# Kernel tuning notes

Hardware: AMD Instinct MI355X
Metric: run time of the kernel (lower is better)

## Reference

```python
import jax, jax.numpy as jnp
import numpy as np

EXPERT_NUM = 8
TOPK = 2
N_EMBD = 768
D_FF = 3072
B, S = 2, 1024
T = B * S


def setup_inputs() -> dict:
    key = jax.random.key(0)
    ks = jax.random.split(key, 6)
    x = jax.random.normal(ks[0], (B, S, N_EMBD), dtype=jnp.float32)
    # gumbel noise, matching gumbel_noise(n, k) in the torch module
    u = jax.random.uniform(ks[1], (T, EXPERT_NUM), dtype=jnp.float32,
                           minval=1e-6, maxval=1.0 - 1e-6)
    noise = -jnp.log(-jnp.log(u))
    router_w = jax.random.normal(ks[2], (EXPERT_NUM, N_EMBD), dtype=jnp.float32) * (N_EMBD ** -0.5)
    w1 = jax.random.normal(ks[3], (EXPERT_NUM, N_EMBD, D_FF), dtype=jnp.float32) * (N_EMBD ** -0.5)
    b1 = jnp.zeros((EXPERT_NUM, D_FF), dtype=jnp.float32)
    w2 = jax.random.normal(ks[4], (EXPERT_NUM, D_FF, N_EMBD), dtype=jnp.float32) * (D_FF ** -0.5)
    b2 = jnp.zeros((EXPERT_NUM, N_EMBD), dtype=jnp.float32)
    return {"x": x, "noise": noise, "router_w": router_w,
            "w1": w1, "b1": b1, "w2": w2, "b2": b2}


def reference(x, noise, router_w, w1, b1, w2, b2):
    d = x.shape[-1]
    xs = x.reshape(-1, d)                                   # [T, d]
    gate_logits = xs @ router_w.T + noise                   # [T, E]
    # topk_exp > 1 branch: topk first, then softmax over the k kept logits
    weights, selected = jax.lax.top_k(gate_logits, TOPK)    # [T, k]
    weights = jax.nn.softmax(weights.astype(jnp.float32), axis=1).astype(x.dtype)
    out = jnp.zeros_like(xs)
    for e in range(EXPERT_NUM):
        # combine weight of expert e per token (0 where not selected)
        w_e = jnp.sum(jnp.where(selected == e, weights, 0.0), axis=1)  # [T]
        h = jax.nn.gelu(xs @ w1[e] + b1[e])                 # [T, d_ff]
        y = h @ w2[e] + b2[e]                               # [T, d]
        out = out + w_e[:, None] * y
    return out.reshape(x.shape)
```

## Files before the change

kernel.cpp:

```cpp
#include <hip/hip_runtime.h>
#include <hip/hip_bf16.h>

#define T_TOK 2048
#define NE 768
#define DFF 3072
#define NEXP 8
#define ROWS_PAD 4480
#define MAX_TILES 40

typedef __attribute__((ext_vector_type(8))) __bf16 bf16x8;
typedef __attribute__((ext_vector_type(4))) __bf16 bf16x4;
typedef __attribute__((ext_vector_type(4))) float f32x4;

__device__ __forceinline__ float gelu_tanh(float v) {
  float u = 0.7978845608028654f * (v + 0.044715f * v * v * v);
  float e = __expf(-2.0f * fabsf(u));
  float t = (1.0f - e) / (1.0f + e);
  t = copysignf(t, u);
  return 0.5f * v * (1.0f + t);
}

__global__ void router_kernel(const float* __restrict__ x,
                              const float* __restrict__ noise,
                              const float* __restrict__ rw,
                              int* __restrict__ sel, float* __restrict__ wgt) {
  int tok  = (blockIdx.x * blockDim.x + threadIdx.x) >> 6;
  int lane = threadIdx.x & 63;
  const float* xr = x + (size_t)tok * NE;
  float acc[NEXP];
#pragma unroll
  for (int e = 0; e < NEXP; e++) acc[e] = 0.f;
  for (int d = lane; d < NE; d += 64) {
    float xv = xr[d];
#pragma unroll
    for (int e = 0; e < NEXP; e++) acc[e] += xv * rw[e * NE + d];
  }
#pragma unroll
  for (int e = 0; e < NEXP; e++) {
#pragma unroll
    for (int off = 32; off > 0; off >>= 1) acc[e] += __shfl_xor(acc[e], off);
  }
  if (lane == 0) {
    float lg[NEXP];
#pragma unroll
    for (int e = 0; e < NEXP; e++) lg[e] = acc[e] + noise[tok * NEXP + e];
    int i0 = 0;
#pragma unroll
    for (int e = 1; e < NEXP; e++) if (lg[e] > lg[i0]) i0 = e;
    int i1 = (i0 == 0) ? 1 : 0;
#pragma unroll
    for (int e = 0; e < NEXP; e++) if (e != i0 && lg[e] > lg[i1]) i1 = e;
    float ex = __expf(lg[i1] - lg[i0]);
    float w0 = 1.f / (1.f + ex);
    sel[tok * 2]     = i0; sel[tok * 2 + 1] = i1;
    wgt[tok * 2]     = w0; wgt[tok * 2 + 1] = 1.f - w0;
  }
}

__global__ void assign_kernel(const int* __restrict__ sel,
                              int* __restrict__ offs, int* __restrict__ pair_tok,
                              int* __restrict__ slot_of, int* __restrict__ tiles,
                              int* __restrict__ ntl) {
  __shared__ int scnt[NEXP];
  __shared__ int soff[NEXP + 1];
  int e = threadIdx.x >> 6;
  int lane = threadIdx.x & 63;

  int count = 0;
  for (int t0 = 0; t0 < T_TOK; t0 += 64) {
    int t = t0 + lane;
    bool m = (sel[t * 2] == e) | (sel[t * 2 + 1] == e);
    count += __popcll(__ballot(m));
  }
  if (lane == 0) scnt[e] = count;
  __syncthreads();

  if (threadIdx.x == 0) {
    int s = 0;
    for (int k = 0; k < NEXP; k++) { soff[k] = s; s += scnt[k]; }
    soff[NEXP] = s;
    for (int i = 0; i <= NEXP; i++) offs[i] = soff[i];
    int k2 = 0;
    for (int k = 0; k < NEXP; k++)
      for (int r = soff[k]; r < soff[k + 1]; r += 128) {
        tiles[k2 * 2] = k; tiles[k2 * 2 + 1] = r; k2++;
      }
    *ntl = k2;
  }
  __syncthreads();

  int base = soff[e];
  for (int t0 = 0; t0 < T_TOK; t0 += 64) {
    int t = t0 + lane;
    int s0 = sel[t * 2], s1 = sel[t * 2 + 1];
    bool m0 = (s0 == e), m1 = (s1 == e);
    bool m = m0 | m1;
    unsigned long long mask = __ballot(m);
    int pos = __popcll(mask & ((1ull << lane) - 1ull));
    if (m) {
      int slot = base + pos;
      pair_tok[slot] = t;
      slot_of[t * 2 + (m0 ? 0 : 1)] = slot;
    }
    base += __popcll(mask);
  }
}

__global__ void gather_kernel(const float* __restrict__ x, const int* __restrict__ pair_tok,
                              __hip_bfloat16* __restrict__ xg) {
  int r = blockIdx.x;
  int tok = pair_tok[r];
  const float4* s = (const float4*)(x + (size_t)tok * NE);
  __hip_bfloat16* d = xg + (size_t)r * NE;
  int t = threadIdx.x;
  if (t < NE / 4) {
    float4 v = s[t];
    bf16x4 o;
    o[0] = (__bf16)__float2bfloat16(v.x); o[1] = (__bf16)__float2bfloat16(v.y);
    o[2] = (__bf16)__float2bfloat16(v.z); o[3] = (__bf16)__float2bfloat16(v.w);
    *reinterpret_cast<bf16x4*>(&d[t * 4]) = o;
  }
}

__global__ void transpose_cvt(const float* __restrict__ src, __hip_bfloat16* __restrict__ dst,
                              int K, int N) {
  __shared__ __hip_bfloat16 tile[64 * 72];
  int ntk = K >> 6, ntn = N >> 6;
  int bid = blockIdx.x;
  int e = bid / (ntk * ntn);
  int rem = bid % (ntk * ntn);
  int tk = rem / ntn, tn = rem % ntn;
  const float* s = src + (size_t)e * K * N + (size_t)(tk * 64) * N + tn * 64;
  int t = threadIdx.x;
  int a = t & 15;
  int kp = t >> 4;
#pragma unroll
  for (int i = 0; i < 2; i++) {
    int k = 2 * kp + 32 * i;
    float4 v0 = *reinterpret_cast<const float4*>(&s[(size_t)k * N + 4 * a]);
    float4 v1 = *reinterpret_cast<const float4*>(&s[(size_t)(k + 1) * N + 4 * a]);
    const float* p0 = &v0.x; const float* p1 = &v1.x;
#pragma unroll
    for (int j = 0; j < 4; j++) {
      __hip_bfloat162 p;
      p.x = __float2bfloat16(p0[j]); p.y = __float2bfloat16(p1[j]);
      *reinterpret_cast<__hip_bfloat162*>(&tile[(4 * a + j) * 72 + k]) = p;
    }
  }
  __syncthreads();
  int n = t >> 3, g = t & 7;
  __hip_bfloat16* d = dst + (size_t)e * N * K + (size_t)(tn * 64) * K + tk * 64;
#pragma unroll
  for (int i = 0; i < 2; i++) {
    int row = n + 32 * i;
    bf16x8 v = *reinterpret_cast<const bf16x8*>(&tile[row * 72 + g * 8]);
    *reinterpret_cast<bf16x8*>(&d[(size_t)row * K + g * 8]) = v;
  }
}

template <int K, int N, int MODE, int SPLITS>
__global__ __launch_bounds__(256) void ffn_gemm(
    const __hip_bfloat16* __restrict__ A, const __hip_bfloat16* __restrict__ Bt,
    const float* __restrict__ bias, __hip_bfloat16* __restrict__ DST,
    const int* __restrict__ offs, const int* __restrict__ tiles,
    const int* __restrict__ ntl) {
  constexpr int NT = N / 128;
  constexpr int KS = K / SPLITS;
  constexpr int NS = KS / 64;
  int bid = blockIdx.x;
  int nt = bid % NT;
  int r1 = bid / NT;
  int sp = r1 % SPLITS;
  int ti = r1 / SPLITS;
  if (ti >= *ntl) return;
  int e = tiles[ti * 2], row0 = tiles[ti * 2 + 1];
  int rend = offs[e + 1];
  int n0 = nt * 128;
  int kbeg = sp * KS;

  __shared__ __align__(16) __hip_bfloat16 lds[2][2][128 * 64];

  int tid = threadIdx.x;
  int w = tid >> 6, l = tid & 63;
  int wr = w >> 1, wc = w & 1;
  int r16 = l & 15, q = l >> 4;
  int swz = r16 & 7;

  f32x4 acc[4][4];
#pragma unroll
  for (int m = 0; m < 4; m++)
#pragma unroll
    for (int n = 0; n < 4; n++) acc[m][n] = (f32x4){0.f, 0.f, 0.f, 0.f};

  const __hip_bfloat16* Bte = Bt + (size_t)e * N * K;

  auto STAGE = [&](int b, int k0) {
    char* cA = (char*)lds[b][0];
    char* cB = (char*)lds[b][1];
#pragma unroll
    for (int i = 0; i < 4; i++) {
      int c = tid + 256 * i;
      int row = c >> 3, p = c & 7;
      const __hip_bfloat16* ga =
          A + (size_t)(row0 + row) * K + k0 + ((p ^ (row & 7)) << 3);
      __builtin_amdgcn_global_load_lds(
          (const __attribute__((address_space(1))) void*)ga,
          (__attribute__((address_space(3))) void*)(cA + c * 16), 16, 0, 0);
    }
#pragma unroll
    for (int i = 0; i < 4; i++) {
      int c = tid + 256 * i;
      int row = c >> 3, p = c & 7;
      const __hip_bfloat16* gb =
          Bte + (size_t)(n0 + row) * K + k0 + ((p ^ (row & 7)) << 3);
      __builtin_amdgcn_global_load_lds(
          (const __attribute__((address_space(1))) void*)gb,
          (__attribute__((address_space(3))) void*)(cB + c * 16), 16, 0, 0);
    }
  };

  STAGE(0, kbeg);
  for (int t = 0; t < NS; t++) {
    if (t + 1 < NS) {
      STAGE((t + 1) & 1, kbeg + (t + 1) * 64);
      asm volatile("s_waitcnt vmcnt(8)" ::: "memory");
    } else {
      asm volatile("s_waitcnt vmcnt(0)" ::: "memory");
    }
    __builtin_amdgcn_s_barrier();
    __builtin_amdgcn_sched_barrier(0);
    const char* cA = (const char*)lds[t & 1][0];
    const char* cB = (const char*)lds[t & 1][1];
#pragma unroll
    for (int kk = 0; kk < 2; kk++) {
      int inner = ((kk * 4 + q) ^ swz) << 4;
      bf16x8 aF[4], bF[4];
#pragma unroll
      for (int m = 0; m < 4; m++)
        aF[m] = *reinterpret_cast<const bf16x8*>(cA + (wr * 64 + m * 16 + r16) * 128 + inner);
#pragma unroll
      for (int n = 0; n < 4; n++)
        bF[n] = *reinterpret_cast<const bf16x8*>(cB + (wc * 64 + n * 16 + r16) * 128 + inner);
#pragma unroll
      for (int m = 0; m < 4; m++)
#pragma unroll
        for (int n = 0; n < 4; n++)
          acc[m][n] = __builtin_amdgcn_mfma_f32_16x16x32_bf16(aF[m], bF[n], acc[m][n], 0, 0, 0);
    }
    __builtin_amdgcn_s_barrier();
  }

  float* ldsF = (float*)&lds[0][0][0];
  __hip_bfloat16* dst = DST + (size_t)sp * ROWS_PAD * N;
#pragma unroll
  for (int hh = 0; hh < 2; hh++) {
    __syncthreads();
    if (wr == hh) {
#pragma unroll
      for (int m = 0; m < 4; m++)
#pragma unroll
        for (int n = 0; n < 4; n++)
#pragma unroll
          for (int rg = 0; rg < 4; rg++)
            ldsF[(m * 16 + q * 4 + rg) * 132 + wc * 64 + n * 16 + r16] = acc[m][n][rg];
    }
    __syncthreads();
#pragma unroll
    for (int i = 0; i < 4; i++) {
      int s = tid + 256 * i;
      int r = s >> 4, c8 = s & 15;
      int rr = row0 + hh * 64 + r;
      if (rr < rend) {
        const float* src = &ldsF[r * 132 + c8 * 8];
        float4 v0 = *reinterpret_cast<const float4*>(src);
        float4 v1 = *reinterpret_cast<const float4*>(src + 4);
        const float* bp = &bias[e * N + n0 + c8 * 8];
        float4 bb0 = *reinterpret_cast<const float4*>(bp);
        float4 bb1 = *reinterpret_cast<const float4*>(bp + 4);
        float vv[8]  = {v0.x, v0.y, v0.z, v0.w, v1.x, v1.y, v1.z, v1.w};
        float bbv[8] = {bb0.x, bb0.y, bb0.z, bb0.w, bb1.x, bb1.y, bb1.z, bb1.w};
        bf16x8 o;
#pragma unroll
        for (int j = 0; j < 8; j++) {
          float val;
          if (MODE == 0) val = gelu_tanh(vv[j] + bbv[j]);
          else           val = vv[j] + (sp == 0 ? bbv[j] : 0.f);
          o[j] = (__bf16)__float2bfloat16(val);
        }
        *reinterpret_cast<bf16x8*>(&dst[(size_t)rr * N + n0 + c8 * 8]) = o;
      }
    }
  }
}

template <int SPLITS>
__global__ void combine_kernel(const __hip_bfloat16* __restrict__ yb,
                               const int* __restrict__ slot_of,
                               const float* __restrict__ wgt,
                               float* __restrict__ out) {
  int t = blockIdx.x;
  int d = threadIdx.x;
  int s0 = slot_of[2 * t], s1 = slot_of[2 * t + 1];
  float w0 = wgt[2 * t], w1 = wgt[2 * t + 1];
  float a0 = 0.f, a1 = 0.f, a2 = 0.f, a3 = 0.f;
#pragma unroll
  for (int sp = 0; sp < SPLITS; sp++) {
    bf16x4 p = reinterpret_cast<const bf16x4*>(yb + (size_t)(sp * ROWS_PAD + s0) * NE)[d];
    bf16x4 r = reinterpret_cast<const bf16x4*>(yb + (size_t)(sp * ROWS_PAD + s1) * NE)[d];
    a0 += w0 * (float)p[0] + w1 * (float)r[0];
    a1 += w0 * (float)p[1] + w1 * (float)r[1];
    a2 += w0 * (float)p[2] + w1 * (float)r[2];
    a3 += w0 * (float)p[3] + w1 * (float)r[3];
  }
  float4 o = {a0, a1, a2, a3};
  reinterpret_cast<float4*>(out)[(size_t)t * (NE / 4) + d] = o;
}

extern "C" void kernel_launch(void* const* d_in, const int* in_sizes, int n_in,
                              void* d_out, int out_size, void* d_ws, size_t ws_size,
                              hipStream_t stream) {
  const float* x     = (const float*)d_in[0];
  const float* noise = (const float*)d_in[1];
  const float* rw    = (const float*)d_in[2];
  const float* w1    = (const float*)d_in[3];
  const float* b1    = (const float*)d_in[4];
  const float* w2    = (const float*)d_in[5];
  const float* b2    = (const float*)d_in[6];
  float* out = (float*)d_out;

  constexpr int SP2 = 4;

  char* ws = (char*)d_ws;
  size_t off = 0;
  auto carve = [&](size_t bytes) { void* p = ws + off; off = (off + bytes + 255) & ~255ull; return p; };
  int*   offs     = (int*)carve((NEXP + 1) * 4);
  int*   sel      = (int*)carve(T_TOK * 2 * 4);
  float* wgt      = (float*)carve(T_TOK * 2 * 4);
  int*   pair_tok = (int*)carve(ROWS_PAD * 4);
  int*   slot_of  = (int*)carve(T_TOK * 2 * 4);
  int*   tiles    = (int*)carve(MAX_TILES * 2 * 4);
  int*   ntl      = (int*)carve(4);
  __hip_bfloat16* xg  = (__hip_bfloat16*)carve((size_t)ROWS_PAD * NE * 2);
  __hip_bfloat16* h   = (__hip_bfloat16*)carve((size_t)ROWS_PAD * DFF * 2);
  __hip_bfloat16* yb  = (__hip_bfloat16*)carve((size_t)SP2 * ROWS_PAD * NE * 2);
  __hip_bfloat16* wt  = (__hip_bfloat16*)carve((size_t)NEXP * NE * DFF * 2);

  hipMemsetAsync(d_out, 0, (size_t)out_size * sizeof(float), stream);
  if (off > ws_size) return;

  router_kernel<<<(T_TOK * 64) / 256, 256, 0, stream>>>(x, noise, rw, sel, wgt);
  assign_kernel<<<1, 512, 0, stream>>>(sel, offs, pair_tok, slot_of, tiles, ntl);
  gather_kernel<<<T_TOK * 2, 256, 0, stream>>>(x, pair_tok, xg);

  transpose_cvt<<<NEXP * (NE / 64) * (DFF / 64), 256, 0, stream>>>(w1, wt, NE, DFF);
  ffn_gemm<NE, DFF, 0, 1><<<MAX_TILES * 1 * (DFF / 128), 256, 0, stream>>>(
      xg, wt, b1, h, offs, tiles, ntl);

  transpose_cvt<<<NEXP * (DFF / 64) * (NE / 64), 256, 0, stream>>>(w2, wt, DFF, NE);
  ffn_gemm<DFF, NE, 1, SP2><<<MAX_TILES * SP2 * (NE / 128), 256, 0, stream>>>(
      h, wt, b2, yb, offs, tiles, ntl);

  combine_kernel<SP2><<<T_TOK, 192, 0, stream>>>(yb, slot_of, wgt, out);
}
```

Before: 159.0 us.

## Switch FFN GEMM to triple-buffered 32-wide K stages, halve split-K

The grouped FFN GEMM now stages 32-wide K slices into a 3-deep LDS ring with an XOR chunk swizzle, where it used to stage 64-wide slices into a double buffer. This keeps two loads in flight per iteration to hide global latency while keeping LDS usage about the same. Split-K for the second GEMM drops from 4 to 2, which means less partial-sum traffic in combine but fewer blocks. The output memset now runs only on the early-exit path, because combine already writes every output element. Each iteration does half the MFMA work, so barrier overhead per FLOP doubles.

```diff
diff --git a/kernel.cpp b/kernel.cpp
--- a/kernel.cpp
+++ b/kernel.cpp
@@ -158,6 +158,10 @@
   }
 }
 
+__device__ __forceinline__ int swz_chunk(int c) {
+  return (c & ~7) | ((c & 7) ^ ((c >> 3) & 7));
+}
+
 template <int K, int N, int MODE, int SPLITS>
 __global__ __launch_bounds__(256) void ffn_gemm(
     const __hip_bfloat16* __restrict__ A, const __hip_bfloat16* __restrict__ Bt,
@@ -166,7 +170,7 @@
     const int* __restrict__ ntl) {
   constexpr int NT = N / 128;
   constexpr int KS = K / SPLITS;
-  constexpr int NS = KS / 64;
+  constexpr int NS = KS / 32;
   int bid = blockIdx.x;
   int nt = bid % NT;
   int r1 = bid / NT;
@@ -178,13 +182,12 @@
   int n0 = nt * 128;
   int kbeg = sp * KS;
 
-  __shared__ __align__(16) __hip_bfloat16 lds[2][2][128 * 64];
+  __shared__ __align__(16) __hip_bfloat16 lds[3][2][128 * 32];
 
   int tid = threadIdx.x;
   int w = tid >> 6, l = tid & 63;
   int wr = w >> 1, wc = w & 1;
   int r16 = l & 15, q = l >> 4;
-  int swz = r16 & 7;
 
   f32x4 acc[4][4];
 #pragma unroll
@@ -198,55 +201,58 @@
     char* cA = (char*)lds[b][0];
     char* cB = (char*)lds[b][1];
 #pragma unroll
-    for (int i = 0; i < 4; i++) {
-      int c = tid + 256 * i;
-      int row = c >> 3, p = c & 7;
-      const __hip_bfloat16* ga =
-          A + (size_t)(row0 + row) * K + k0 + ((p ^ (row & 7)) << 3);
+    for (int i = 0; i < 2; i++) {
+      int Lc = tid + 256 * i;
+      int fc = swz_chunk(Lc);
+      int row = fc >> 2, p = fc & 3;
+      const __hip_bfloat16* ga = A + (size_t)(row0 + row) * K + k0 + p * 8;
       __builtin_amdgcn_global_load_lds(
           (const __attribute__((address_space(1))) void*)ga,
-          (__attribute__((address_space(3))) void*)(cA + c * 16), 16, 0, 0);
-    }
-#pragma unroll
-    for (int i = 0; i < 4; i++) {
-      int c = tid + 256 * i;
-      int row = c >> 3, p = c & 7;
-      const __hip_bfloat16* gb =
-          Bte + (size_t)(n0 + row) * K + k0 + ((p ^ (row & 7)) << 3);
+          (__attribute__((address_space(3))) void*)(cA + Lc * 16), 16, 0, 0);
+    }
+#pragma unroll
+    for (int i = 0; i < 2; i++) {
+      int Lc = tid + 256 * i;
+      int fc = swz_chunk(Lc);
+      int row = fc >> 2, p = fc & 3;
+      const __hip_bfloat16* gb = Bte + (size_t)(n0 + row) * K + k0 + p * 8;
       __builtin_amdgcn_global_load_lds(
           (const __attribute__((address_space(1))) void*)gb,
-          (__attribute__((address_space(3))) void*)(cB + c * 16), 16, 0, 0);
+          (__attribute__((address_space(3))) void*)(cB + Lc * 16), 16, 0, 0);
     }
   };
 
   STAGE(0, kbeg);
+  if (NS > 1) STAGE(1, kbeg + 32);
   for (int t = 0; t < NS; t++) {
-    if (t + 1 < NS) {
-      STAGE((t + 1) & 1, kbeg + (t + 1) * 64);
+    if (t + 2 < NS) {
+      STAGE((t + 2) % 3, kbeg + (t + 2) * 32);
       asm volatile("s_waitcnt vmcnt(8)" ::: "memory");
+    } else if (t + 1 < NS) {
+      asm volatile("s_waitcnt vmcnt(4)" ::: "memory");
     } else {
       asm volatile("s_waitcnt vmcnt(0)" ::: "memory");
     }
     __builtin_amdgcn_s_barrier();
     __builtin_amdgcn_sched_barrier(0);
-    const char* cA = (const char*)lds[t & 1][0];
-    const char* cB = (const char*)lds[t & 1][1];
-#pragma unroll
-    for (int kk = 0; kk < 2; kk++) {
-      int inner = ((kk * 4 + q) ^ swz) << 4;
-      bf16x8 aF[4], bF[4];
-#pragma unroll
-      for (int m = 0; m < 4; m++)
-        aF[m] = *reinterpret_cast<const bf16x8*>(cA + (wr * 64 + m * 16 + r16) * 128 + inner);
+    const char* cA = (const char*)lds[t % 3][0];
+    const char* cB = (const char*)lds[t % 3][1];
+    bf16x8 aF[4], bF[4];
+#pragma unroll
+    for (int m = 0; m < 4; m++) {
+      int row = wr * 64 + m * 16 + r16;
+      aF[m] = *reinterpret_cast<const bf16x8*>(cA + swz_chunk(row * 4 + q) * 16);
+    }
+#pragma unroll
+    for (int n = 0; n < 4; n++) {
+      int row = wc * 64 + n * 16 + r16;
+      bF[n] = *reinterpret_cast<const bf16x8*>(cB + swz_chunk(row * 4 + q) * 16);
+    }
+#pragma unroll
+    for (int m = 0; m < 4; m++)
 #pragma unroll
       for (int n = 0; n < 4; n++)
-        bF[n] = *reinterpret_cast<const bf16x8*>(cB + (wc * 64 + n * 16 + r16) * 128 + inner);
-#pragma unroll
-      for (int m = 0; m < 4; m++)
-#pragma unroll
-        for (int n = 0; n < 4; n++)
-          acc[m][n] = __builtin_amdgcn_mfma_f32_16x16x32_bf16(aF[m], bF[n], acc[m][n], 0, 0, 0);
-    }
+        acc[m][n] = __builtin_amdgcn_mfma_f32_16x16x32_bf16(aF[m], bF[n], acc[m][n], 0, 0, 0);
     __builtin_amdgcn_s_barrier();
   }
 
@@ -328,7 +334,7 @@
   const float* b2    = (const float*)d_in[6];
   float* out = (float*)d_out;
 
-  constexpr int SP2 = 4;
+  constexpr int SP2 = 2;
 
   char* ws = (char*)d_ws;
   size_t off = 0;
@@ -345,8 +351,10 @@
   __hip_bfloat16* yb  = (__hip_bfloat16*)carve((size_t)SP2 * ROWS_PAD * NE * 2);
   __hip_bfloat16* wt  = (__hip_bfloat16*)carve((size_t)NEXP * NE * DFF * 2);
 
-  hipMemsetAsync(d_out, 0, (size_t)out_size * sizeof(float), stream);
-  if (off > ws_size) return;
+  if (off > ws_size) {
+    hipMemsetAsync(d_out, 0, (size_t)out_size * sizeof(float), stream);
+    return;
+  }
 
   router_kernel<<<(T_TOK * 64) / 256, 256, 0, stream>>>(x, noise, rw, sel, wgt);
   assign_kernel<<<1, 512, 0, stream>>>(sel, offs, pair_tok, slot_of, tiles, ntl);
```

Result: faster. 154.7 us, median of 2 (-2.7%).
